# Performance work log

Measured on AMD Instinct MI355X. Metric: run time of the kernel, lower is better.

## Reference

```python
import jax, jax.numpy as jnp
import numpy as np


def _conv1d(x, w, b):
    # x: [N, Cin, L], w: [Cout, Cin, 3], padding=1 (same)
    y = jax.lax.conv_general_dilated(x, w, (1,), ((1, 1),),
                                     dimension_numbers=('NCH', 'OIH', 'NCH'))
    return y + b[None, :, None]


def _pool2(x):
    n, c, l = x.shape
    return x.reshape(n, c, l // 2, 2).max(-1)


def _forward(x, w_init, b_init, c1w, c1b, c2w, c2b, c3w, c3b,
             Wx, bx, Wh, bh, Wxo, bxo, Wq, bq, Wk, bk, Wv, bv,
             Wao, bao, Wout, bout):
    B, MEL, T = x.shape
    H = Wxo.shape[0]
    D = Wao.shape[1]
    # --- FeatureExtractor ---
    f = jnp.transpose(x, (0, 2, 1))                 # [B,T,MEL]
    f = jax.nn.relu(f @ w_init.T + b_init)          # [B,T,4L]
    f = f.reshape(B * T, 1, -1)                     # [B*T,1,4L]
    f = _pool2(jax.nn.relu(_conv1d(f, c1w, c1b)))   # [B*T,16,2L]
    f = _pool2(jax.nn.relu(_conv1d(f, c2w, c2b)))   # [B*T,32,L]
    f = _conv1d(f, c3w, c3b)                        # [B*T,1,L] (no relu after conv3)
    f = f.reshape(B, T, -1)                         # [B,T,L]
    scale = 1.0 / jnp.sqrt(jnp.asarray(D, x.dtype))
    def step(carry, x_t):
        c, h = carry
        # fused gate computation: g-order = (i, f, g, o)
        g = (jnp.einsum('gol,bl->bgo', Wx, x_t) + bx
             + jnp.einsum('goh,bh->bgo', Wh, h) + bh)  # [B,4,H]
        i_g = jax.nn.sigmoid(g[:, 0])
        f_g = jax.nn.sigmoid(g[:, 1])
        g_g = jnp.tanh(g[:, 2])
        o_g = jax.nn.sigmoid(g[:, 3])
        c = f_g * c + i_g * g_g
        x_o = jax.nn.sigmoid(x_t @ Wxo.T + bxo)       # [B,H]
        q = (x_o @ Wq.T + bq).reshape(B, H, D)
        k = (c @ Wk.T + bk).reshape(B, H, D)
        v = (o_g @ Wv.T + bv).reshape(B, H, D)
        attn = jax.nn.softmax(jnp.einsum('bhd,bgd->bhg', q, k) * scale, axis=-1)
        ao = jnp.einsum('bhg,bgd->bhd', attn, v)      # [B,H,D]
        h = ao @ Wao[0] + bao[0]                      # [B,H]
        y = h @ Wout.T + bout                         # [B,C]
        return (c, h), y
    c0 = jnp.zeros((B, H), x.dtype)
    h0 = jnp.zeros((B, H), x.dtype)
    _, ys = jax.lax.scan(step, (c0, h0), jnp.transpose(f, (1, 0, 2)))  # [T,B,C]
    return jnp.transpose(ys, (1, 2, 0))               # [B,C,T]


def setup_inputs() -> dict:
    key = jax.random.key(0)
    ks = jax.random.split(key, 16)
    B, MEL, T, L, H, C, D = 8, 128, 64, 256, 256, 10, 256
    s = 0.02
    inp = {}
    inp['x'] = jax.random.normal(ks[0], (B, MEL, T), jnp.float32)
    inp['w_init'] = jax.random.normal(ks[1], (4 * L, MEL), jnp.float32) * s
    inp['b_init'] = jnp.zeros((4 * L,), jnp.float32)
    inp['c1w'] = jax.random.normal(ks[2], (16, 1, 3), jnp.float32) * s
    inp['c1b'] = jnp.zeros((16,), jnp.float32)
    inp['c2w'] = jax.random.normal(ks[3], (32, 16, 3), jnp.float32) * s
    inp['c2b'] = jnp.zeros((32,), jnp.float32)
    inp['c3w'] = jax.random.normal(ks[4], (1, 32, 3), jnp.float32) * s
    inp['c3b'] = jnp.zeros((1,), jnp.float32)
    inp['Wx'] = jax.random.normal(ks[5], (4, H, L), jnp.float32) * s
    inp['bx'] = jnp.zeros((4, H), jnp.float32)
    inp['Wh'] = jax.random.normal(ks[6], (4, H, H), jnp.float32) * s
    inp['bh'] = jnp.zeros((4, H), jnp.float32)
    inp['Wxo'] = jax.random.normal(ks[7], (H, L), jnp.float32) * s
    inp['bxo'] = jnp.zeros((H,), jnp.float32)
    inp['Wq'] = jax.random.normal(ks[8], (H * D, H), jnp.float32) * s
    inp['bq'] = jnp.zeros((H * D,), jnp.float32)
    inp['Wk'] = jax.random.normal(ks[9], (H * D, H), jnp.float32) * s
    inp['bk'] = jnp.zeros((H * D,), jnp.float32)
    inp['Wv'] = jax.random.normal(ks[10], (H * D, H), jnp.float32) * s
    inp['bv'] = jnp.zeros((H * D,), jnp.float32)
    inp['Wao'] = jax.random.normal(ks[11], (1, D), jnp.float32) * s
    inp['bao'] = jnp.zeros((1,), jnp.float32)
    inp['Wout'] = jax.random.normal(ks[12], (C, H), jnp.float32) * s
    inp['bout'] = jnp.zeros((C,), jnp.float32)
    return inp


def reference(x, w_init, b_init, c1w, c1b, c2w, c2b, c3w, c3b,
              Wx, bx, Wh, bh, Wxo, bxo, Wq, bq, Wk, bk, Wv, bv,
              Wao, bao, Wout, bout):
    return _forward(x, w_init, b_init, c1w, c1b, c2w, c2b, c3w, c3b,
                    Wx, bx, Wh, bh, Wxo, bxo, Wq, bq, Wk, bk, Wv, bv,
                    Wao, bao, Wout, bout)
```

## Files before the change

### kernel.cpp

```cpp
#include <hip/hip_runtime.h>
#include <hip/hip_fp16.h>
#include <math.h>

#define WS_XIN   0L
#define WS_GF    65536L
#define WS_STATS 65536L
#define WS_BARS  98304L
#define WS_FS    589824L
#define WS_XO    720896L
#define WS_GX    851968L
#define WS_Q     1376256L
#define WS_WKH   18153472L
#define WS_WVE   34930688L
#define WS_BVE   34996224L
#define WS_KT    34996480L
#define WS_HH    35520768L
#define WS_C     35653888L
#define WS_OG    35655936L
#define WS_VW    35657984L

#define NBLK 256

typedef unsigned long long u64;

__device__ __forceinline__ float sigmf(float x){ return 1.0f/(1.0f + expf(-x)); }
__device__ __forceinline__ float dot4(float4 a, float4 b){
  return a.x*b.x + a.y*b.y + a.z*b.z + a.w*b.w;
}
__device__ __forceinline__ void h8_to_f8(uint4 v, float4& a, float4& b){
  const __half2* hp = (const __half2*)&v;
  float2 f0 = __half22float2(hp[0]);
  float2 f1 = __half22float2(hp[1]);
  float2 f2 = __half22float2(hp[2]);
  float2 f3 = __half22float2(hp[3]);
  a = make_float4(f0.x, f0.y, f1.x, f1.y);
  b = make_float4(f2.x, f2.y, f3.x, f3.y);
}
__device__ __forceinline__ float4 h4_to_f4(uint2 v){
  const __half2* hp = (const __half2*)&v;
  float2 f0 = __half22float2(hp[0]);
  float2 f1 = __half22float2(hp[1]);
  return make_float4(f0.x, f0.y, f1.x, f1.y);
}

__device__ __forceinline__ float cld(const float* p){
  return __hip_atomic_load((float*)p, __ATOMIC_RELAXED, __HIP_MEMORY_SCOPE_AGENT);
}
__device__ __forceinline__ void cst(float* p, float v){
  __hip_atomic_store(p, v, __ATOMIC_RELAXED, __HIP_MEMORY_SCOPE_AGENT);
}
__device__ __forceinline__ float2 cld2(const float* p){
  u64 v = __hip_atomic_load((const u64*)p, __ATOMIC_RELAXED, __HIP_MEMORY_SCOPE_AGENT);
  float2 r;
  r.x = __uint_as_float((unsigned)(v & 0xffffffffu));
  r.y = __uint_as_float((unsigned)(v >> 32));
  return r;
}
__device__ __forceinline__ void cst2(float* p, float a, float b){
  u64 v = ((u64)__float_as_uint(b) << 32) | (u64)__float_as_uint(a);
  __hip_atomic_store((u64*)p, v, __ATOMIC_RELAXED, __HIP_MEMORY_SCOPE_AGENT);
}

__device__ __forceinline__ void gbar(unsigned* bar, unsigned ph){
  __syncthreads();
  if (threadIdx.x == 0){
    const unsigned g = blockIdx.x & 31u;
    asm volatile("s_waitcnt vmcnt(0)" ::: "memory");
    unsigned old = __hip_atomic_fetch_add(&bar[g*64], 1u, __ATOMIC_RELAXED, __HIP_MEMORY_SCOPE_AGENT);
    if (old == ph*8u - 1u){
      unsigned t = __hip_atomic_fetch_add(&bar[2048], 1u, __ATOMIC_RELAXED, __HIP_MEMORY_SCOPE_AGENT);
      if (t == ph*32u - 1u)
        __hip_atomic_store(&bar[2112], ph, __ATOMIC_RELAXED, __HIP_MEMORY_SCOPE_AGENT);
    }
    if (blockIdx.x < 32){
      while (__hip_atomic_load(&bar[2112], __ATOMIC_RELAXED, __HIP_MEMORY_SCOPE_AGENT) < ph)
        __builtin_amdgcn_s_sleep(2);
      __hip_atomic_store(&bar[2176 + blockIdx.x*64], ph, __ATOMIC_RELAXED, __HIP_MEMORY_SCOPE_AGENT);
    } else {
      while (__hip_atomic_load(&bar[2176 + g*64], __ATOMIC_RELAXED, __HIP_MEMORY_SCOPE_AGENT) < ph)
        __builtin_amdgcn_s_sleep(2);
    }
  }
  __syncthreads();
}

__launch_bounds__(256)
__global__ void k_init(const float* __restrict__ x, float* __restrict__ ws){
  int i = blockIdx.x*256 + threadIdx.x;
  int r = i >> 7, m = i & 127;
  int t = r >> 3, b = r & 7;
  ws[WS_XIN + i] = x[b*8192 + m*64 + t];
  if (i < 2048){ ws[WS_HH + i] = 0.f; ws[WS_C + i] = 0.f; }
}

__launch_bounds__(256)
__global__ void k_wk16(const float* __restrict__ in, __half* __restrict__ out){
  size_t i = ((size_t)blockIdx.x*256 + threadIdx.x)*8;
  float4 a = *(const float4*)(in + i);
  float4 b = *(const float4*)(in + i + 4);
  uint4 v;
  __half2* vp = (__half2*)&v;
  vp[0] = __floats2half2_rn(a.x, a.y);
  vp[1] = __floats2half2_rn(a.z, a.w);
  vp[2] = __floats2half2_rn(b.x, b.y);
  vp[3] = __floats2half2_rn(b.z, b.w);
  *(uint4*)(out + i) = v;
}

__launch_bounds__(256)
__global__ void k_gemm_nt(const float* __restrict__ W, const float* __restrict__ X,
                          const float* __restrict__ b1, const float* __restrict__ b2,
                          float* __restrict__ out, int M, int K, int act){
  __shared__ float Wt[32*132];
  __shared__ float Xt[32*132];
  const int tid = threadIdx.x;
  const int tx = tid & 15, ty = tid >> 4;
  const int m0 = blockIdx.x * 128, n0 = blockIdx.y * 128;
  float acc[8][8];
  #pragma unroll
  for (int i = 0; i < 8; i++)
    #pragma unroll
    for (int j = 0; j < 8; j++) acc[i][j] = 0.f;

  for (int k0 = 0; k0 < K; k0 += 32){
    #pragma unroll
    for (int i = 0; i < 4; i++){
      int f4 = i*256 + tid;
      int row = f4 >> 3;
      int j4 = (f4 & 7) * 4;
      float4 w = *(const float4*)&W[(size_t)(m0+row)*K + k0 + j4];
      Wt[(j4+0)*132 + row] = w.x;
      Wt[(j4+1)*132 + row] = w.y;
      Wt[(j4+2)*132 + row] = w.z;
      Wt[(j4+3)*132 + row] = w.w;
      float4 xv = *(const float4*)&X[(size_t)(n0+row)*K + k0 + j4];
      Xt[(j4+0)*132 + row] = xv.x;
      Xt[(j4+1)*132 + row] = xv.y;
      Xt[(j4+2)*132 + row] = xv.z;
      Xt[(j4+3)*132 + row] = xv.w;
    }
    __syncthreads();
    for (int k = 0; k < 32; k++){
      float4 a0 = *(const float4*)&Wt[k*132 + 4*tx];
      float4 a1 = *(const float4*)&Wt[k*132 + 64 + 4*tx];
      float4 x0 = *(const float4*)&Xt[k*132 + 4*ty];
      float4 x1 = *(const float4*)&Xt[k*132 + 64 + 4*ty];
      float am[8] = {a0.x,a0.y,a0.z,a0.w,a1.x,a1.y,a1.z,a1.w};
      float xn[8] = {x0.x,x0.y,x0.z,x0.w,x1.x,x1.y,x1.z,x1.w};
      #pragma unroll
      for (int mi = 0; mi < 8; mi++)
        #pragma unroll
        for (int ni = 0; ni < 8; ni++)
          acc[mi][ni] += am[mi]*xn[ni];
    }
    __syncthreads();
  }

  float bvv[8];
  #pragma unroll
  for (int mi = 0; mi < 8; mi++){
    int m = m0 + ((mi < 4) ? (4*tx + mi) : (64 + 4*tx + mi - 4));
    float bb = b1[m];
    if (b2) bb += b2[m];
    bvv[mi] = bb;
  }
  #pragma unroll
  for (int ni = 0; ni < 8; ni++){
    int n = n0 + ((ni < 4) ? (4*ty + ni) : (64 + 4*ty + ni - 4));
    float v[8];
    #pragma unroll
    for (int mi = 0; mi < 8; mi++){
      float q = acc[mi][ni] + bvv[mi];
      if (act == 1) q = fmaxf(q, 0.f);
      else if (act == 2) q = 1.0f/(1.0f + expf(-q));
      v[mi] = q;
    }
    if (act == 3){
      __half* outh = (__half*)out;
      uint2 u0, u1;
      __half2* up0 = (__half2*)&u0;
      __half2* up1 = (__half2*)&u1;
      up0[0] = __floats2half2_rn(v[0], v[1]);
      up0[1] = __floats2half2_rn(v[2], v[3]);
      up1[0] = __floats2half2_rn(v[4], v[5]);
      up1[1] = __floats2half2_rn(v[6], v[7]);
      *(uint2*)&outh[(size_t)n*M + m0 + 4*tx]      = u0;
      *(uint2*)&outh[(size_t)n*M + m0 + 64 + 4*tx] = u1;
    } else {
      *(float4*)&out[(size_t)n*M + m0 + 4*tx]      = make_float4(v[0],v[1],v[2],v[3]);
      *(float4*)&out[(size_t)n*M + m0 + 64 + 4*tx] = make_float4(v[4],v[5],v[6],v[7]);
    }
  }
}

__launch_bounds__(256)
__global__ void k_feconv(const float* __restrict__ gf, const float* __restrict__ c1w,
                         const float* __restrict__ c1b, const float* __restrict__ c2w,
                         const float* __restrict__ c2b, const float* __restrict__ c3w,
                         const float* __restrict__ c3b, float* __restrict__ fs){
  __shared__ float fc[1024];
  __shared__ float p1[16*512];
  __shared__ float p2[32*256];
  __shared__ float w1[48], w2[1536], w3[96], bb1[16], bb2[32];
  const int r = blockIdx.x, tid = threadIdx.x;
  #pragma unroll
  for (int i = 0; i < 4; i++) fc[i*256 + tid] = gf[(size_t)r*1024 + i*256 + tid];
  if (tid < 48) w1[tid] = c1w[tid];
  if (tid < 16) bb1[tid] = c1b[tid];
  for (int i = tid; i < 1536; i += 256) w2[i] = c2w[i];
  if (tid < 32) bb2[tid] = c2b[tid];
  if (tid < 96) w3[tid] = c3w[tid];
  __syncthreads();
  for (int i = 0; i < 32; i++){
    int idx = i*256 + tid;
    int ch = idx >> 9, p = idx & 511;
    float k0 = w1[ch*3], k1 = w1[ch*3+1], k2 = w1[ch*3+2], bias = bb1[ch];
    int q = 2*p;
    float xm1 = (q >= 1) ? fc[q-1] : 0.f;
    float x0 = fc[q];
    float x1 = fc[q+1];
    float x2 = (q+2 < 1024) ? fc[q+2] : 0.f;
    float a0 = bias + k0*xm1 + k1*x0 + k2*x1;
    float a1 = bias + k0*x0 + k1*x1 + k2*x2;
    p1[ch*512 + p] = fmaxf(fmaxf(a0, 0.f), fmaxf(a1, 0.f));
  }
  __syncthreads();
  for (int i = 0; i < 32; i++){
    int idx = i*256 + tid;
    int ch = idx >> 8, p = idx & 255;
    float a0 = bb2[ch], a1 = bb2[ch];
    int q = 2*p;
    #pragma unroll
    for (int ci = 0; ci < 16; ci++){
      const float* wp = &w2[(ch*16+ci)*3];
      const float* ip = &p1[ci*512];
      float xm1 = (q >= 1) ? ip[q-1] : 0.f;
      float x0 = ip[q];
      float x1 = ip[q+1];
      float x2 = (q+2 < 512) ? ip[q+2] : 0.f;
      a0 += wp[0]*xm1 + wp[1]*x0 + wp[2]*x1;
      a1 += wp[0]*x0  + wp[1]*x1 + wp[2]*x2;
    }
    p2[ch*256 + p] = fmaxf(fmaxf(a0, 0.f), fmaxf(a1, 0.f));
  }
  __syncthreads();
  if (tid < 256){
    float a = c3b[0];
    const int l = tid;
    #pragma unroll
    for (int ci = 0; ci < 32; ci++){
      const float* wp = &w3[ci*3];
      const float* ip = &p2[ci*256];
      float xm1 = (l >= 1) ? ip[l-1] : 0.f;
      float x0 = ip[l];
      float x2 = (l+1 < 256) ? ip[l+1] : 0.f;
      a += wp[0]*xm1 + wp[1]*x0 + wp[2]*x2;
    }
    fs[(size_t)r*256 + l] = a;
  }
}

__launch_bounds__(256)
__global__ void k_wveff(const float* __restrict__ Wv, const float* __restrict__ bvq,
                        const float* __restrict__ Wao, float* __restrict__ wve,
                        float* __restrict__ bve, unsigned* __restrict__ bar){
  __shared__ float wa[256];
  const int g = blockIdx.x, tid = threadIdx.x;
  if (g == 0){
    for (int i = tid; i < 8192; i += 256) bar[i] = 0u;
  }
  wa[tid] = Wao[tid];
  __syncthreads();
  float acc = 0.f;
  for (int d = 0; d < 256; d++)
    acc += Wv[((size_t)(g*256 + d))*256 + tid] * wa[d];
  wve[g*256 + tid] = acc;
  if (tid == 0){
    float s = 0.f;
    for (int d = 0; d < 256; d++) s += bvq[g*256 + d]*wa[d];
    bve[g] = s;
  }
}

__global__ __launch_bounds__(512, 2)
void k_loop(const float* __restrict__ gx, const float* __restrict__ Wh,
            const __half* __restrict__ wkh, const float* __restrict__ bkb,
            const float* __restrict__ wve, const float* __restrict__ bve,
            const __half* __restrict__ Qh, const float* __restrict__ bao,
            const float* __restrict__ Wout, const float* __restrict__ bout,
            float* __restrict__ c, float* __restrict__ og, float* __restrict__ vw,
            float* __restrict__ Kt, float* __restrict__ stats, float* __restrict__ hH,
            float* __restrict__ y, unsigned* __restrict__ bar){
  __shared__ float S[25088];
  const int blk = blockIdx.x, tid = threadIdx.x;
  unsigned ph = 0;
  const float bao0 = bao[0];

  const int p1_b = blk >> 5, p1_s = blk & 31;
  const int gid  = blk;
  const int p3_b = blk >> 5, p3_ht = (blk >> 2) & 7, p3_gt = blk & 3;
  const int p3_h0 = p3_ht*32, p3_g0 = p3_gt*64;

  float4 whr[4];
  int p1_row;
  {
    const int j = tid >> 4, part = tid & 15;
    const int rr = p1_s*32 + j, o = rr >> 2, gate = rr & 3;
    p1_row = gate*256 + o;
    const float4* wr = (const float4*)(Wh + (size_t)p1_row*256);
    #pragma unroll
    for (int u = 0; u < 4; u++) whr[u] = wr[u*16 + part];
  }

  for (int t = 0; t < 64; t++){
    if (t > 0){
      if (tid < 256){
        const float* sp = stats + ((size_t)p1_b*256 + tid)*16;
        float2 a0 = cld2(sp+0);  float2 b0 = cld2(sp+2);
        float2 a1 = cld2(sp+4);  float2 b1 = cld2(sp+6);
        float2 a2 = cld2(sp+8);  float2 b2 = cld2(sp+10);
        float2 a3 = cld2(sp+12); float2 b3 = cld2(sp+14);
        float m = fmaxf(fmaxf(a0.x, a1.x), fmaxf(a2.x, a3.x));
        float e0 = expf(a0.x - m), e1 = expf(a1.x - m), e2 = expf(a2.x - m), e3 = expf(a3.x - m);
        float den = a0.y*e0 + a1.y*e1 + a2.y*e2 + a3.y*e3;
        float num = b0.x*e0 + b1.x*e1 + b2.x*e2 + b3.x*e3;
        float hv = num/den + bao0;
        S[tid] = hv;
        if (p1_s == 0) cst(&hH[(size_t)t*2048 + p1_b*256 + tid], hv);
      }
    } else {
      if (tid < 256) S[tid] = 0.f;
    }
    __syncthreads();
    {
      const int j = tid >> 4, part = tid & 15;
      const float4* h4 = (const float4*)S;
      float a0 = 0.f;
      #pragma unroll
      for (int u = 0; u < 4; u++)
        a0 += dot4(whr[u], h4[u*16 + part]);
      a0 += __shfl_xor(a0, 1);
      a0 += __shfl_xor(a0, 2);
      a0 += __shfl_xor(a0, 4);
      a0 += __shfl_xor(a0, 8);
      if (part == 0) S[256 + j] = a0 + gx[(size_t)(t*8 + p1_b)*1024 + p1_row];
    }
    __syncthreads();
    if (tid < 8){
      const int o_ = p1_s*8 + tid, ci = p1_b*256 + o_;
      float ig = sigmf(S[256 + tid*4 + 0]);
      float fg = sigmf(S[256 + tid*4 + 1]);
      float gg = tanhf(S[256 + tid*4 + 2]);
      float ov = sigmf(S[256 + tid*4 + 3]);
      float cv = cld(&c[ci]);
      cst(&c[ci], fg*cv + ig*gg);
      cst(&og[ci], ov);
    }
    gbar(bar, ++ph);

    {
      int bb0 = tid >> 6, j40 = tid & 63;
      float* dst = &S[bb0*260 + j40*4];
      const float* src = &c[bb0*256 + j40*4];
      float2 v0 = cld2(src);
      float2 v1 = cld2(src+2);
      dst[0] = v0.x; dst[1] = v0.y; dst[2] = v1.x; dst[3] = v1.y;
    }
    __syncthreads();
    if (tid < 64){
      const int bb = tid >> 3, part = tid & 7;
      const float4* wv4 = (const float4*)(wve + gid*256);
      float sacc = 0.f;
      #pragma unroll
      for (int u = 0; u < 8; u++){
        float4 w = wv4[part*8 + u];
        const float* op = &og[bb*256 + (part*8 + u)*4];
        float2 o0 = cld2(op);
        float2 o1 = cld2(op+2);
        sacc += w.x*o0.x + w.y*o0.y + w.z*o1.x + w.w*o1.y;
      }
      sacc += __shfl_xor(sacc, 1);
      sacc += __shfl_xor(sacc, 2);
      sacc += __shfl_xor(sacc, 4);
      if (part == 0) cst(&vw[bb*256 + gid], sacc + bve[gid]);
    }
    {
      const float4* cl4 = (const float4*)S;
      #pragma unroll 4
      for (int p = 0; p < 8; p++){
        const int d = p*32 + (tid >> 4), part = tid & 15;
        const __half* wr = wkh + ((size_t)gid*256 + d)*256;
        float4 w0 = h4_to_f4(*(const uint2*)(wr + part*4));
        float4 w1 = h4_to_f4(*(const uint2*)(wr + 64 + part*4));
        float4 w2 = h4_to_f4(*(const uint2*)(wr + 128 + part*4));
        float4 w3 = h4_to_f4(*(const uint2*)(wr + 192 + part*4));
        float acc[8];
        #pragma unroll
        for (int bb = 0; bb < 8; bb++){
          acc[bb] = dot4(w0, cl4[bb*65 + part]) + dot4(w1, cl4[bb*65 + 16 + part])
                  + dot4(w2, cl4[bb*65 + 32 + part]) + dot4(w3, cl4[bb*65 + 48 + part]);
        }
        #pragma unroll
        for (int bb = 0; bb < 8; bb++){
          acc[bb] += __shfl_xor(acc[bb], 1);
          acc[bb] += __shfl_xor(acc[bb], 2);
          acc[bb] += __shfl_xor(acc[bb], 4);
          acc[bb] += __shfl_xor(acc[bb], 8);
        }
        const float bkv = bkb[gid*256 + d];
        if (part < 8)
          cst(&Kt[(size_t)part*65536 + gid*256 + d], acc[part] + bkv);
      }
    }
    gbar(bar, ++ph);

    {
      const __half* Qb = Qh + ((size_t)(t*8 + p3_b))*65536 + (size_t)p3_h0*256;
      #pragma unroll
      for (int i = 0; i < 2; i++){
        int f8 = i*512 + tid;
        int hh = f8 >> 5, j8 = f8 & 31;
        uint4 v = *(const uint4*)(Qb + hh*256 + j8*8);
        float4 a, b;
        h8_to_f8(v, a, b);
        float* dst = &S[hh*260 + j8*8];
        *(float4*)dst = a;
        *(float4*)(dst+4) = b;
      }
      const float* Kb = Kt + (size_t)p3_b*65536 + (size_t)p3_g0*256;
      float* Kl = S + 8320;
      #pragma unroll
      for (int i = 0; i < 8; i++){
        int f4 = i*512 + tid;
        int gg = f4 >> 6, j4 = (f4 & 63)*4;
        float* dst = &Kl[gg*260 + j4];
        const float* src = &Kb[gg*256 + j4];
        float2 v0 = cld2(src);
        float2 v1 = cld2(src+2);
        dst[0] = v0.x; dst[1] = v0.y; dst[2] = v1.x; dst[3] = v1.y;
      }
      if (tid < 64) S[24960 + tid] = cld(&vw[p3_b*256 + p3_g0 + tid]);
      __syncthreads();
      const int kh = tid >> 7, r = tid & 127, ty = r >> 4, txl = r & 15;
      float acc[4][4];
      #pragma unroll
      for (int a = 0; a < 4; a++)
        #pragma unroll
        for (int i = 0; i < 4; i++) acc[a][i] = 0.f;
      const float4* Ql4 = (const float4*)S;
      const float4* Kl4 = (const float4*)(S + 8320);
      for (int k4 = 0; k4 < 16; k4++){
        const int kk = kh*16 + k4;
        float4 qv[4], kv[4];
        #pragma unroll
        for (int a = 0; a < 4; a++) qv[a] = Ql4[(ty + 8*a)*65 + kk];
        #pragma unroll
        for (int i = 0; i < 4; i++) kv[i] = Kl4[(txl + 16*i)*65 + kk];
        #pragma unroll
        for (int a = 0; a < 4; a++)
          #pragma unroll
          for (int i = 0; i < 4; i++)
            acc[a][i] += dot4(qv[a], kv[i]);
      }
      __syncthreads();
      float* Pl = S;
      if (kh > 0){
        #pragma unroll
        for (int a = 0; a < 4; a++)
          #pragma unroll
          for (int i = 0; i < 4; i++)
            Pl[(kh-1)*2048 + r*16 + a*4 + i] = acc[a][i];
      }
      __syncthreads();
      if (kh == 0){
        #pragma unroll
        for (int p = 0; p < 3; p++)
          #pragma unroll
          for (int a = 0; a < 4; a++)
            #pragma unroll
            for (int i = 0; i < 4; i++)
              acc[a][i] += Pl[p*2048 + r*16 + a*4 + i];
        #pragma unroll
        for (int a = 0; a < 4; a++)
          #pragma unroll
          for (int i = 0; i < 4; i++)
            acc[a][i] *= 0.0625f;
        #pragma unroll
        for (int a = 0; a < 4; a++){
          float mx = fmaxf(fmaxf(acc[a][0], acc[a][1]), fmaxf(acc[a][2], acc[a][3]));
          mx = fmaxf(mx, __shfl_xor(mx, 1));
          mx = fmaxf(mx, __shfl_xor(mx, 2));
          mx = fmaxf(mx, __shfl_xor(mx, 4));
          mx = fmaxf(mx, __shfl_xor(mx, 8));
          float den = 0.f, num = 0.f;
          #pragma unroll
          for (int i = 0; i < 4; i++){
            float pv = expf(acc[a][i] - mx);
            den += pv;
            num += pv * S[24960 + txl + 16*i];
          }
          den += __shfl_xor(den, 1); num += __shfl_xor(num, 1);
          den += __shfl_xor(den, 2); num += __shfl_xor(num, 2);
          den += __shfl_xor(den, 4); num += __shfl_xor(num, 4);
          den += __shfl_xor(den, 8); num += __shfl_xor(num, 8);
          if (txl == 0){
            const int h = p3_h0 + ty + 8*a;
            float* sp = &stats[(((size_t)p3_b*256 + h)*4 + p3_gt)*4];
            cst2(sp, mx, den);
            cst(sp+2, num);
          }
        }
      }
    }
    gbar(bar, ++ph);
  }

  if (p1_s == 0 && tid < 256){
    const float* sp = stats + ((size_t)p1_b*256 + tid)*16;
    float2 a0 = cld2(sp+0);  float2 b0 = cld2(sp+2);
    float2 a1 = cld2(sp+4);  float2 b1 = cld2(sp+6);
    float2 a2 = cld2(sp+8);  float2 b2 = cld2(sp+10);
    float2 a3 = cld2(sp+12); float2 b3 = cld2(sp+14);
    float m = fmaxf(fmaxf(a0.x, a1.x), fmaxf(a2.x, a3.x));
    float e0 = expf(a0.x - m), e1 = expf(a1.x - m), e2 = expf(a2.x - m), e3 = expf(a3.x - m);
    float den = a0.y*e0 + a1.y*e1 + a2.y*e2 + a3.y*e3;
    float num = b0.x*e0 + b1.x*e1 + b2.x*e2 + b3.x*e3;
    cst(&hH[(size_t)64*2048 + p1_b*256 + tid], num/den + bao0);
  }
  gbar(bar, ++ph);
  if (blk < 64 && tid < 80){
    const int t2 = blk;
    const int bb2 = tid/10, cc = tid - bb2*10;
    const float* hr = &hH[(size_t)(t2+1)*2048 + bb2*256];
    const float* wr2 = &Wout[cc*256];
    float acc = 0.f;
    for (int u = 0; u < 128; u++){
      float2 h2 = cld2(hr + u*2);
      acc += h2.x*wr2[u*2] + h2.y*wr2[u*2+1];
    }
    y[bb2*640 + cc*64 + t2] = acc + bout[cc];
  }
}

extern "C" void kernel_launch(void* const* d_in, const int* in_sizes, int n_in,
                              void* d_out, int out_size, void* d_ws, size_t ws_size,
                              hipStream_t stream){
  (void)in_sizes; (void)n_in; (void)out_size; (void)ws_size;
  const float* x      = (const float*)d_in[0];
  const float* w_init = (const float*)d_in[1];
  const float* b_init = (const float*)d_in[2];
  const float* c1w    = (const float*)d_in[3];
  const float* c1b    = (const float*)d_in[4];
  const float* c2w    = (const float*)d_in[5];
  const float* c2b    = (const float*)d_in[6];
  const float* c3w    = (const float*)d_in[7];
  const float* c3b    = (const float*)d_in[8];
  const float* Wx     = (const float*)d_in[9];
  const float* bx     = (const float*)d_in[10];
  const float* Wh     = (const float*)d_in[11];
  const float* bh     = (const float*)d_in[12];
  const float* Wxo    = (const float*)d_in[13];
  const float* bxo    = (const float*)d_in[14];
  const float* Wq     = (const float*)d_in[15];
  const float* bq     = (const float*)d_in[16];
  const float* Wk     = (const float*)d_in[17];
  const float* bk_    = (const float*)d_in[18];
  const float* Wv     = (const float*)d_in[19];
  const float* bv     = (const float*)d_in[20];
  const float* Wao    = (const float*)d_in[21];
  const float* bao    = (const float*)d_in[22];
  const float* Wout   = (const float*)d_in[23];
  const float* bout   = (const float*)d_in[24];
  float* y  = (float*)d_out;
  float* ws = (float*)d_ws;

  float* xin   = ws + WS_XIN;
  float* gf    = ws + WS_GF;
  float* stats = ws + WS_STATS;
  unsigned* bar = (unsigned*)(ws + WS_BARS);
  float* fs    = ws + WS_FS;
  float* xo    = ws + WS_XO;
  float* gxp   = ws + WS_GX;
  __half* Qh   = (__half*)(ws + WS_Q);
  __half* wkh  = (__half*)(ws + WS_WKH);
  float* wve   = ws + WS_WVE;
  float* bve   = ws + WS_BVE;
  float* Ktp   = ws + WS_KT;
  float* hH    = ws + WS_HH;
  float* cp    = ws + WS_C;
  float* ogp   = ws + WS_OG;
  float* vwp   = ws + WS_VW;

  k_init<<<256, 256, 0, stream>>>(x, ws);
  k_wk16<<<8192, 256, 0, stream>>>(Wk, wkh);
  k_gemm_nt<<<dim3(8, 4), 256, 0, stream>>>(w_init, xin, b_init, nullptr, gf, 1024, 128, 1);
  k_feconv<<<512, 256, 0, stream>>>(gf, c1w, c1b, c2w, c2b, c3w, c3b, fs);
  k_gemm_nt<<<dim3(2, 4), 256, 0, stream>>>(Wxo, fs, bxo, nullptr, xo, 256, 256, 2);
  k_gemm_nt<<<dim3(8, 4), 256, 0, stream>>>(Wx, fs, bx, bh, gxp, 1024, 256, 0);
  k_wveff<<<256, 256, 0, stream>>>(Wv, bv, Wao, wve, bve, bar);
  k_gemm_nt<<<dim3(512, 4), 256, 0, stream>>>(Wq, xo, bq, nullptr, (float*)Qh, 65536, 256, 3);
  k_loop<<<NBLK, 512, 0, stream>>>(gxp, Wh, wkh, bk_, wve, bve, Qh, bao, Wout, bout,
                                   cp, ogp, vwp, Ktp, stats, hH, y, bar);
}
```

Before: 2.557 ms.

## Use fp16 dot2 GEMM for Q projection and per-batch barrier in loop

Converts Wq to fp16 and replaces the large Q-projection GEMM with a new kernel using packed half dot2 instructions over fp16-staged tiles. It also swaps one grid-wide barrier in the recurrent loop for a per-batch barrier over the 32 blocks sharing a batch, and lowers an unroll factor in the K-projection loop. This aims to cut FP32 FMA work in the Q GEMM and global synchronisation latency per step. It risks precision loss from fp16 inputs and adds an extra Wq conversion pass over a large weight.

```diff
diff --git a/kernel.cpp b/kernel.cpp
--- a/kernel.cpp
+++ b/kernel.cpp
@@ -11,6 +11,7 @@
 #define WS_GX    851968L
 #define WS_Q     1376256L
 #define WS_WKH   18153472L
+#define WS_WQH   26542080L
 #define WS_WVE   34930688L
 #define WS_BVE   34996224L
 #define WS_KT    34996480L
@@ -22,6 +23,7 @@
 #define NBLK 256
 
 typedef unsigned long long u64;
+typedef _Float16 h2v __attribute__((ext_vector_type(2)));
 
 __device__ __forceinline__ float sigmf(float x){ return 1.0f/(1.0f + expf(-x)); }
 __device__ __forceinline__ float dot4(float4 a, float4 b){
@@ -42,6 +44,17 @@
   float2 f1 = __half22float2(hp[1]);
   return make_float4(f0.x, f0.y, f1.x, f1.y);
 }
+__device__ __forceinline__ float fdot2c(__half2 a, __half2 b, float c){
+#if __has_builtin(__builtin_amdgcn_fdot2)
+  h2v av = *(h2v*)&a;
+  h2v bv = *(h2v*)&b;
+  return __builtin_amdgcn_fdot2(av, bv, c, false);
+#else
+  float2 af = __half22float2(a);
+  float2 bf = __half22float2(b);
+  return fmaf(af.y, bf.y, fmaf(af.x, bf.x, c));
+#endif
+}
 
 __device__ __forceinline__ float cld(const float* p){
   return __hip_atomic_load((float*)p, __ATOMIC_RELAXED, __HIP_MEMORY_SCOPE_AGENT);
@@ -80,6 +93,18 @@
       while (__hip_atomic_load(&bar[2176 + g*64], __ATOMIC_RELAXED, __HIP_MEMORY_SCOPE_AGENT) < ph)
         __builtin_amdgcn_s_sleep(2);
     }
+  }
+  __syncthreads();
+}
+
+__device__ __forceinline__ void bbar(unsigned* bar, int b, unsigned phb){
+  __syncthreads();
+  if (threadIdx.x == 0){
+    unsigned* cnt = &bar[6144 + b*64];
+    asm volatile("s_waitcnt vmcnt(0)" ::: "memory");
+    __hip_atomic_fetch_add(cnt, 1u, __ATOMIC_RELAXED, __HIP_MEMORY_SCOPE_AGENT);
+    while (__hip_atomic_load(cnt, __ATOMIC_RELAXED, __HIP_MEMORY_SCOPE_AGENT) < phb*32u)
+      __builtin_amdgcn_s_sleep(2);
   }
   __syncthreads();
 }
@@ -175,21 +200,84 @@
       else if (act == 2) q = 1.0f/(1.0f + expf(-q));
       v[mi] = q;
     }
-    if (act == 3){
-      __half* outh = (__half*)out;
-      uint2 u0, u1;
-      __half2* up0 = (__half2*)&u0;
-      __half2* up1 = (__half2*)&u1;
-      up0[0] = __floats2half2_rn(v[0], v[1]);
-      up0[1] = __floats2half2_rn(v[2], v[3]);
-      up1[0] = __floats2half2_rn(v[4], v[5]);
-      up1[1] = __floats2half2_rn(v[6], v[7]);
-      *(uint2*)&outh[(size_t)n*M + m0 + 4*tx]      = u0;
-      *(uint2*)&outh[(size_t)n*M + m0 + 64 + 4*tx] = u1;
-    } else {
-      *(float4*)&out[(size_t)n*M + m0 + 4*tx]      = make_float4(v[0],v[1],v[2],v[3]);
-      *(float4*)&out[(size_t)n*M + m0 + 64 + 4*tx] = make_float4(v[4],v[5],v[6],v[7]);
-    }
+    *(float4*)&out[(size_t)n*M + m0 + 4*tx]      = make_float4(v[0],v[1],v[2],v[3]);
+    *(float4*)&out[(size_t)n*M + m0 + 64 + 4*tx] = make_float4(v[4],v[5],v[6],v[7]);
+  }
+}
+
+__launch_bounds__(256)
+__global__ void k_gemmq(const __half* __restrict__ Wh, const float* __restrict__ X,
+                        const float* __restrict__ b1, __half* __restrict__ out){
+  __shared__ __half2 Wt[16*132];
+  __shared__ __half2 Xt[16*132];
+  const int tid = threadIdx.x;
+  const int tx = tid & 15, ty = tid >> 4;
+  const int m0 = blockIdx.x * 128, n0 = blockIdx.y * 128;
+  float acc[8][8];
+  #pragma unroll
+  for (int i = 0; i < 8; i++)
+    #pragma unroll
+    for (int j = 0; j < 8; j++) acc[i][j] = 0.f;
+
+  for (int k0 = 0; k0 < 256; k0 += 32){
+    #pragma unroll
+    for (int i = 0; i < 2; i++){
+      int f = i*256 + tid;
+      int row = f >> 2, q = f & 3;
+      uint4 wv = *(const uint4*)(Wh + (size_t)(m0+row)*256 + k0 + q*8);
+      const __half2* wp = (const __half2*)&wv;
+      #pragma unroll
+      for (int j = 0; j < 4; j++)
+        Wt[(q*4 + j)*132 + row] = wp[j];
+    }
+    #pragma unroll
+    for (int i = 0; i < 4; i++){
+      int f = i*256 + tid;
+      int row = f >> 3, q = f & 7;
+      float4 xv = *(const float4*)&X[(size_t)(n0+row)*256 + k0 + q*4];
+      Xt[(q*2    )*132 + row] = __floats2half2_rn(xv.x, xv.y);
+      Xt[(q*2 + 1)*132 + row] = __floats2half2_rn(xv.z, xv.w);
+    }
+    __syncthreads();
+    for (int k2 = 0; k2 < 16; k2++){
+      __half2 am[8], xn[8];
+      #pragma unroll
+      for (int s = 0; s < 4; s++){
+        am[s]   = Wt[k2*132 + 4*tx + s];
+        am[4+s] = Wt[k2*132 + 64 + 4*tx + s];
+        xn[s]   = Xt[k2*132 + 4*ty + s];
+        xn[4+s] = Xt[k2*132 + 64 + 4*ty + s];
+      }
+      #pragma unroll
+      for (int mi = 0; mi < 8; mi++)
+        #pragma unroll
+        for (int ni = 0; ni < 8; ni++)
+          acc[mi][ni] = fdot2c(am[mi], xn[ni], acc[mi][ni]);
+    }
+    __syncthreads();
+  }
+
+  float bvv[8];
+  #pragma unroll
+  for (int mi = 0; mi < 8; mi++){
+    int m = m0 + ((mi < 4) ? (4*tx + mi) : (64 + 4*tx + mi - 4));
+    bvv[mi] = b1[m];
+  }
+  #pragma unroll
+  for (int ni = 0; ni < 8; ni++){
+    int n = n0 + ((ni < 4) ? (4*ty + ni) : (64 + 4*ty + ni - 4));
+    float v[8];
+    #pragma unroll
+    for (int mi = 0; mi < 8; mi++) v[mi] = acc[mi][ni] + bvv[mi];
+    uint2 u0, u1;
+    __half2* up0 = (__half2*)&u0;
+    __half2* up1 = (__half2*)&u1;
+    up0[0] = __floats2half2_rn(v[0], v[1]);
+    up0[1] = __floats2half2_rn(v[2], v[3]);
+    up1[0] = __floats2half2_rn(v[4], v[5]);
+    up1[1] = __floats2half2_rn(v[6], v[7]);
+    *(uint2*)&out[(size_t)n*65536 + m0 + 4*tx]      = u0;
+    *(uint2*)&out[(size_t)n*65536 + m0 + 64 + 4*tx] = u1;
   }
 }
 
@@ -293,7 +381,7 @@
             float* __restrict__ y, unsigned* __restrict__ bar){
   __shared__ float S[25088];
   const int blk = blockIdx.x, tid = threadIdx.x;
-  unsigned ph = 0;
+  unsigned ph = 0, phb = 0;
   const float bao0 = bao[0];
 
   const int p1_b = blk >> 5, p1_s = blk & 31;
@@ -386,7 +474,7 @@
     }
     {
       const float4* cl4 = (const float4*)S;
-      #pragma unroll 4
+      #pragma unroll 2
       for (int p = 0; p < 8; p++){
         const int d = p*32 + (tid >> 4), part = tid & 15;
         const __half* wr = wkh + ((size_t)gid*256 + d)*256;
@@ -512,7 +600,7 @@
         }
       }
     }
-    gbar(bar, ++ph);
+    bbar(bar, p3_b, ++phb);
   }
 
   if (p1_s == 0 && tid < 256){
@@ -583,6 +671,7 @@
   float* gxp   = ws + WS_GX;
   __half* Qh   = (__half*)(ws + WS_Q);
   __half* wkh  = (__half*)(ws + WS_WKH);
+  __half* wqh  = (__half*)(ws + WS_WQH);
   float* wve   = ws + WS_WVE;
   float* bve   = ws + WS_BVE;
   float* Ktp   = ws + WS_KT;
@@ -593,12 +682,13 @@
 
   k_init<<<256, 256, 0, stream>>>(x, ws);
   k_wk16<<<8192, 256, 0, stream>>>(Wk, wkh);
+  k_wk16<<<8192, 256, 0, stream>>>(Wq, wqh);
   k_gemm_nt<<<dim3(8, 4), 256, 0, stream>>>(w_init, xin, b_init, nullptr, gf, 1024, 128, 1);
   k_feconv<<<512, 256, 0, stream>>>(gf, c1w, c1b, c2w, c2b, c3w, c3b, fs);
   k_gemm_nt<<<dim3(2, 4), 256, 0, stream>>>(Wxo, fs, bxo, nullptr, xo, 256, 256, 2);
   k_gemm_nt<<<dim3(8, 4), 256, 0, stream>>>(Wx, fs, bx, bh, gxp, 1024, 256, 0);
   k_wveff<<<256, 256, 0, stream>>>(Wv, bv, Wao, wve, bve, bar);
-  k_gemm_nt<<<dim3(512, 4), 256, 0, stream>>>(Wq, xo, bq, nullptr, (float*)Qh, 65536, 256, 3);
+  k_gemmq<<<dim3(512, 4), 256, 0, stream>>>(wqh, xo, bq, Qh);
   k_loop<<<NBLK, 512, 0, stream>>>(gxp, Wh, wkh, bk_, wve, bve, Qh, bao, Wout, bout,
                                    cp, ogp, vwp, Ktp, stats, hH, y, bar);
 }
```

Result: faster. 2.477 ms (-3.1%).
